# Kernel optimization log

Hardware: AMD Instinct MI355X
Metric: run time of the kernel (lower is better)

## Reference

```python
import jax, jax.numpy as jnp
import numpy as np

EPS = 1e-6


def setup_inputs() -> dict:
    key = jax.random.key(0)
    kq, kk, kv = jax.random.split(key, 3)
    B, H, S, D = 1, 16, 2048, 64
    q = jax.random.normal(kq, (B, H, S, D), dtype=jnp.float32)
    k = jax.random.normal(kk, (B, H, S, D), dtype=jnp.float32)
    v = jax.random.normal(kv, (B, H, S, D), dtype=jnp.float32)
    return {"q": q, "k": k, "v": v}


def reference(q, k, v):
    # Rebased linear attention: squared scaled QK score, causal mask,
    # normalized by running row-sum (not softmax).
    B, H, S, D = q.shape
    scale = D ** (-0.5)
    # [B,H,S,S] raw scores
    s = jnp.einsum("bhid,bhjd->bhij", q, k) * scale
    s2 = s * s
    causal = jnp.tril(jnp.ones((S, S), dtype=bool))  # k_idx <= q_idx
    s2 = jnp.where(causal, s2, jnp.zeros((), dtype=s2.dtype))
    z = jnp.sum(s2, axis=-1)  # [B,H,S]
    o = jnp.einsum("bhij,bhjd->bhid", s2, v)
    return o / (z[..., None] + EPS)
```

## Files before the change

kernel.cpp:

```cpp
#include <hip/hip_runtime.h>

typedef __attribute__((ext_vector_type(8))) short bf16x8;
typedef __attribute__((ext_vector_type(16))) float f32x16;

#define SLEN 2048
#define DDIM 64
#define NH 16
#define KEPS 1e-6f
#define TILE_B 16384
#define PSTR 72

__device__ __forceinline__ short f2bf(float x) {
    unsigned u = __float_as_uint(x);
    unsigned r = (u + 0x7FFFu + ((u >> 16) & 1u)) >> 16;
    return (short)r;
}
__device__ __forceinline__ unsigned cvtpk(float lo, float hi) {
    unsigned r;
    asm("v_cvt_pk_bf16_f32 %0, %1, %2" : "=v"(r) : "v"(lo), "v"(hi));
    return r;
}
__device__ __forceinline__ f32x16 mfma32x32(bf16x8 a, bf16x8 b, f32x16 c) {
    return __builtin_amdgcn_mfma_f32_32x32x16_bf16(a, b, c, 0, 0, 0);
}

__global__ void __launch_bounds__(256) prep_kernel(
    const float* __restrict__ K, const float* __restrict__ V, char* __restrict__ WS)
{
    __shared__ short vt[64 * PSTR];
    const int b  = blockIdx.x;
    const int h  = b >> 5;
    const int kt = b & 31;
    const int t  = threadIdx.x;
    const int j  = t >> 2;
    const int ks = t & 3;
    const int c16 = ks * 16;

    char* chunk = WS + (size_t)b * TILE_B;

    {
        const float* src = K + ((size_t)h * SLEN + kt * 64 + j) * DDIM + c16;
        float4 a = ((const float4*)src)[0], bb = ((const float4*)src)[1];
        float4 c = ((const float4*)src)[2], d = ((const float4*)src)[3];
        uint4 lo = make_uint4(cvtpk(a.x,a.y), cvtpk(a.z,a.w), cvtpk(bb.x,bb.y), cvtpk(bb.z,bb.w));
        uint4 hi = make_uint4(cvtpk(c.x,c.y), cvtpk(c.z,c.w), cvtpk(d.x,d.y), cvtpk(d.z,d.w));
        *(uint4*)(chunk + ((size_t)((ks*2+0)*64 + j)) * 16) = lo;
        *(uint4*)(chunk + ((size_t)((ks*2+1)*64 + j)) * 16) = hi;
    }
    {
        const float* src = V + ((size_t)h * SLEN + kt * 64 + j) * DDIM + c16;
        float4 a = ((const float4*)src)[0], bb = ((const float4*)src)[1];
        float4 c = ((const float4*)src)[2], d = ((const float4*)src)[3];
        float f[16] = {a.x,a.y,a.z,a.w, bb.x,bb.y,bb.z,bb.w, c.x,c.y,c.z,c.w, d.x,d.y,d.z,d.w};
#pragma unroll
        for (int q = 0; q < 16; ++q)
            vt[(c16 + q) * PSTR + j] = f2bf(f[q]);
    }
    __syncthreads();
    {
        const int d  = t >> 2;
        const int jc = (t & 3) * 16;
        uint4 lo = *(const uint4*)&vt[d * PSTR + jc];
        uint4 hi = *(const uint4*)&vt[d * PSTR + jc + 8];
        char* vbase = chunk + 8192;
        *(uint4*)(vbase + (size_t)(((jc >> 4) * 2 + 0) * 64 + d) * 16) = lo;
        *(uint4*)(vbase + (size_t)(((jc >> 4) * 2 + 1) * 64 + d) * 16) = hi;
    }
}

__global__ void __launch_bounds__(512, 4) attn_main(
    const float* __restrict__ Q, const char* __restrict__ WS, float* __restrict__ O)
{
    __shared__ float red[2][3][64][33];

    const int bid = blockIdx.x;
    const int xcd = bid & 7;
    const int m   = bid >> 3;
    const int h   = xcd | ((m & 1) << 3);
    const int c   = m >> 1;

    const int tid  = threadIdx.x;
    const int w    = tid >> 6;
    const int lane = tid & 63;
    const int il   = lane & 31;
    const int hi   = lane >> 5;
    const int msel = w >> 2;
    const int jb   = (w >> 1) & 1;
    const int e    = w & 1;

    const int g    = msel ? (31 - c) : c;
    const int half = msel;
    const int q0   = g * 64 + half * 32;

    const float* __restrict__ Qh = Q + (size_t)h * SLEN * DDIM;
    float* __restrict__ Oh = O + (size_t)h * SLEN * DDIM;
    const char* __restrict__ WSh = WS + (size_t)h * 32 * TILE_B;

    bf16x8 qf[4];
#pragma unroll
    for (int ks = 0; ks < 4; ++ks) {
        const float* src = Qh + (size_t)(q0 + il) * DDIM + ks * 16 + hi * 8;
        float4 a = *reinterpret_cast<const float4*>(src);
        float4 b = *reinterpret_cast<const float4*>(src + 4);
        uint4 uq = make_uint4(cvtpk(a.x, a.y), cvtpk(a.z, a.w),
                              cvtpk(b.x, b.y), cvtpk(b.z, b.w));
        qf[ks] = *reinterpret_cast<bf16x8*>(&uq);
    }

    f32x16 oacc0, oacc1;
#pragma unroll
    for (int rr = 0; rr < 16; ++rr) { oacc0[rr] = 0.f; oacc1[rr] = 0.f; }
    float zacc = 0.f;

    const int koff = (hi * 64 + jb * 32 + il) * 16;
    const int voff = 8192 + ((jb * 2 * 2 + hi) * 64 + il) * 16;

    const int ktend = g - ((jb > half) ? 1 : 0);

    if (e <= ktend) {
        const char* kb = WSh + (size_t)e * TILE_B + koff;
        bf16x8 kf0 = *(const bf16x8*)(kb);
        bf16x8 kf1 = *(const bf16x8*)(kb + 2048);
        bf16x8 kf2 = *(const bf16x8*)(kb + 4096);
        bf16x8 kf3 = *(const bf16x8*)(kb + 6144);

        for (int kt = e; kt <= ktend; kt += 2) {
            const char* tb = WSh + (size_t)kt * TILE_B;
            const char* vb = tb + voff;
            bf16x8 v00 = *(const bf16x8*)(vb);
            bf16x8 v01 = *(const bf16x8*)(vb + 512);
            bf16x8 v10 = *(const bf16x8*)(vb + 2048);
            bf16x8 v11 = *(const bf16x8*)(vb + 2560);

            f32x16 s;
#pragma unroll
            for (int rr = 0; rr < 16; ++rr) s[rr] = 0.f;
            s = mfma32x32(kf0, qf[0], s);
            s = mfma32x32(kf1, qf[1], s);
            s = mfma32x32(kf2, qf[2], s);
            s = mfma32x32(kf3, qf[3], s);

            if (kt + 2 <= ktend) {
                const char* nb = WSh + (size_t)(kt + 2) * TILE_B + koff;
                kf0 = *(const bf16x8*)(nb);
                kf1 = *(const bf16x8*)(nb + 2048);
                kf2 = *(const bf16x8*)(nb + 4096);
                kf3 = *(const bf16x8*)(nb + 6144);
            }

            const bool tri = (kt == g) && (jb == half);
#pragma unroll
            for (int rr = 0; rr < 16; ++rr) {
                float x = s[rr];
                x = x * x * 0.015625f;
                if (tri) {
                    int jl = (rr & 3) + 8 * (rr >> 2) + 4 * hi;
                    if (jl > il) x = 0.f;
                }
                s[rr] = x;
            }
            {
                float a0 = (s[0] + s[1]) + (s[2] + s[3]);
                float a1 = (s[4] + s[5]) + (s[6] + s[7]);
                float a2 = (s[8] + s[9]) + (s[10] + s[11]);
                float a3 = (s[12] + s[13]) + (s[14] + s[15]);
                zacc += (a0 + a1) + (a2 + a3);
            }

            {
                unsigned X  = cvtpk(s[0], s[1]);
                unsigned Xp = cvtpk(s[2], s[3]);
                unsigned Y  = cvtpk(s[4], s[5]);
                unsigned Yp = cvtpk(s[6], s[7]);
                asm("v_permlane32_swap_b32 %0, %1" : "+v"(X), "+v"(Y));
                asm("v_permlane32_swap_b32 %0, %1" : "+v"(Xp), "+v"(Yp));
                uint4 aw = make_uint4(X, Xp, Y, Yp);
                bf16x8 pf = *reinterpret_cast<bf16x8*>(&aw);
                oacc0 = mfma32x32(pf, v00, oacc0);
                oacc1 = mfma32x32(pf, v01, oacc1);
            }
            {
                unsigned X  = cvtpk(s[8],  s[9]);
                unsigned Xp = cvtpk(s[10], s[11]);
                unsigned Y  = cvtpk(s[12], s[13]);
                unsigned Yp = cvtpk(s[14], s[15]);
                asm("v_permlane32_swap_b32 %0, %1" : "+v"(X), "+v"(Y));
                asm("v_permlane32_swap_b32 %0, %1" : "+v"(Xp), "+v"(Yp));
                uint4 aw = make_uint4(X, Xp, Y, Yp);
                bf16x8 pf = *reinterpret_cast<bf16x8*>(&aw);
                oacc0 = mfma32x32(pf, v10, oacc0);
                oacc1 = mfma32x32(pf, v11, oacc1);
            }
        }
    }

    zacc += __shfl_xor(zacc, 32);
    const int sw = w & 3;
    if (sw != 0) {
        float* r = &red[msel][sw - 1][lane][0];
#pragma unroll
        for (int rr = 0; rr < 16; ++rr) { r[rr] = oacc0[rr]; r[16 + rr] = oacc1[rr]; }
        r[32] = zacc;
    }
    __syncthreads();
    if (sw == 0) {
#pragma unroll
        for (int pp = 0; pp < 3; ++pp) {
            const float* r = &red[msel][pp][lane][0];
#pragma unroll
            for (int rr = 0; rr < 16; ++rr) { oacc0[rr] += r[rr]; oacc1[rr] += r[16 + rr]; }
            zacc += r[32];
        }
        const float invl = 1.f / (zacc + KEPS);
#pragma unroll
        for (int rr = 0; rr < 16; ++rr) {
            const int rl = (rr & 3) + 8 * (rr >> 2) + 4 * hi;
            const float inv = __shfl(invl, rl);
            Oh[(size_t)(q0 + rl) * DDIM + il]      = oacc0[rr] * inv;
            Oh[(size_t)(q0 + rl) * DDIM + 32 + il] = oacc1[rr] * inv;
        }
    }
}

__global__ void __launch_bounds__(512, 4) attn_fp32(
    const float* __restrict__ Q, const float* __restrict__ K,
    const float* __restrict__ V, float* __restrict__ O)
{
    __shared__ float red[2][3][64][33];

    const int bid = blockIdx.x;
    const int xcd = bid & 7;
    const int m   = bid >> 3;
    const int h   = xcd | ((m & 1) << 3);
    const int c   = m >> 1;

    const int tid  = threadIdx.x;
    const int w    = tid >> 6;
    const int lane = tid & 63;
    const int il   = lane & 31;
    const int hi   = lane >> 5;
    const int msel = w >> 2;
    const int jb   = (w >> 1) & 1;
    const int e    = w & 1;

    const int g    = msel ? (31 - c) : c;
    const int half = msel;
    const int q0   = g * 64 + half * 32;

    const float* Qh = Q + (size_t)h * SLEN * DDIM;
    const float* Kh = K + (size_t)h * SLEN * DDIM;
    const float* Vh = V + (size_t)h * SLEN * DDIM;
    float* Oh = O + (size_t)h * SLEN * DDIM;

    bf16x8 qf[4];
#pragma unroll
    for (int ks = 0; ks < 4; ++ks) {
        const float* src = Qh + (size_t)(q0 + il) * DDIM + ks * 16 + hi * 8;
        float4 a = *reinterpret_cast<const float4*>(src);
        float4 b = *reinterpret_cast<const float4*>(src + 4);
        uint4 uq = make_uint4(cvtpk(a.x, a.y), cvtpk(a.z, a.w),
                              cvtpk(b.x, b.y), cvtpk(b.z, b.w));
        qf[ks] = *reinterpret_cast<bf16x8*>(&uq);
    }

    f32x16 oacc0, oacc1;
#pragma unroll
    for (int rr = 0; rr < 16; ++rr) { oacc0[rr] = 0.f; oacc1[rr] = 0.f; }
    float zacc = 0.f;

    const int ktend = g - ((jb > half) ? 1 : 0);

    for (int kt = e; kt <= ktend; kt += 2) {
        f32x16 s;
#pragma unroll
        for (int rr = 0; rr < 16; ++rr) s[rr] = 0.f;
#pragma unroll
        for (int ks = 0; ks < 4; ++ks) {
            const float* src = Kh + (size_t)(kt * 64 + jb * 32 + il) * DDIM + ks * 16 + hi * 8;
            float4 a = *reinterpret_cast<const float4*>(src);
            float4 b = *reinterpret_cast<const float4*>(src + 4);
            uint4 uk = make_uint4(cvtpk(a.x, a.y), cvtpk(a.z, a.w),
                                  cvtpk(b.x, b.y), cvtpk(b.z, b.w));
            s = mfma32x32(*reinterpret_cast<bf16x8*>(&uk), qf[ks], s);
        }
        const bool tri = (kt == g) && (jb == half);
#pragma unroll
        for (int rr = 0; rr < 16; ++rr) {
            float x = s[rr];
            x = x * x * 0.015625f;
            if (tri) {
                int jl = (rr & 3) + 8 * (rr >> 2) + 4 * hi;
                if (jl > il) x = 0.f;
            }
            s[rr] = x;
            zacc += x;
        }
#pragma unroll
        for (int s16 = 0; s16 < 2; ++s16) {
            unsigned X  = cvtpk(s[8*s16+0], s[8*s16+1]);
            unsigned Xp = cvtpk(s[8*s16+2], s[8*s16+3]);
            unsigned Y  = cvtpk(s[8*s16+4], s[8*s16+5]);
            unsigned Yp = cvtpk(s[8*s16+6], s[8*s16+7]);
            asm("v_permlane32_swap_b32 %0, %1" : "+v"(X), "+v"(Y));
            asm("v_permlane32_swap_b32 %0, %1" : "+v"(Xp), "+v"(Yp));
            uint4 aw = make_uint4(X, Xp, Y, Yp);
            bf16x8 pf = *reinterpret_cast<bf16x8*>(&aw);
#pragma unroll
            for (int dt = 0; dt < 2; ++dt) {
                float v8[8];
#pragma unroll
                for (int t = 0; t < 8; ++t)
                    v8[t] = Vh[(size_t)(kt * 64 + (jb * 2 + s16) * 16 + hi * 8 + t) * DDIM + dt * 32 + il];
                uint4 uv = make_uint4(cvtpk(v8[0], v8[1]), cvtpk(v8[2], v8[3]),
                                      cvtpk(v8[4], v8[5]), cvtpk(v8[6], v8[7]));
                bf16x8 vf = *reinterpret_cast<bf16x8*>(&uv);
                if (dt == 0) oacc0 = mfma32x32(pf, vf, oacc0);
                else         oacc1 = mfma32x32(pf, vf, oacc1);
            }
        }
    }

    zacc += __shfl_xor(zacc, 32);
    const int sw = w & 3;
    if (sw != 0) {
        float* r = &red[msel][sw - 1][lane][0];
#pragma unroll
        for (int rr = 0; rr < 16; ++rr) { r[rr] = oacc0[rr]; r[16 + rr] = oacc1[rr]; }
        r[32] = zacc;
    }
    __syncthreads();
    if (sw == 0) {
#pragma unroll
        for (int pp = 0; pp < 3; ++pp) {
            const float* r = &red[msel][pp][lane][0];
#pragma unroll
            for (int rr = 0; rr < 16; ++rr) { oacc0[rr] += r[rr]; oacc1[rr] += r[16 + rr]; }
            zacc += r[32];
        }
        const float invl = 1.f / (zacc + KEPS);
#pragma unroll
        for (int rr = 0; rr < 16; ++rr) {
            const int rl = (rr & 3) + 8 * (rr >> 2) + 4 * hi;
            const float inv = __shfl(invl, rl);
            Oh[(size_t)(q0 + rl) * DDIM + il]      = oacc0[rr] * inv;
            Oh[(size_t)(q0 + rl) * DDIM + 32 + il] = oacc1[rr] * inv;
        }
    }
}

extern "C" void kernel_launch(void* const* d_in, const int* in_sizes, int n_in,
                              void* d_out, int out_size, void* d_ws, size_t ws_size,
                              hipStream_t stream) {
    const float* q = (const float*)d_in[0];
    const float* k = (const float*)d_in[1];
    const float* v = (const float*)d_in[2];
    float* o = (float*)d_out;

    const size_t need = (size_t)NH * 32 * TILE_B;
    if (ws_size >= need) {
        char* ws = (char*)d_ws;
        hipLaunchKernelGGL(prep_kernel, dim3(NH * 32), dim3(256), 0, stream, k, v, ws);
        hipLaunchKernelGGL(attn_main, dim3(512), dim3(512), 0, stream, q, ws, o);
    } else {
        hipLaunchKernelGGL(attn_fp32, dim3(512), dim3(512), 0, stream, q, k, v, o);
    }
}
```

Before: 30.78 us.

## Process paired query slices sequentially in 256-thread blocks, prefetch V, simplify V transpose

The main kernel now uses 256-thread blocks that handle two balanced query slices (s and 63-s) one after the other, instead of 512 threads splitting them across wave halves. V fragments are now prefetched one tile ahead like K, and s_setprio raises wave priority around the MFMA sections. The prep kernel drops its LDS transpose and builds packed V pairs directly from four row loads. Each block now carries the same work with fewer waves, so there is less parallelism per CU and a second reduction barrier per block.

```diff
diff --git a/kernel.cpp b/kernel.cpp
--- a/kernel.cpp
+++ b/kernel.cpp
@@ -8,13 +8,7 @@
 #define NH 16
 #define KEPS 1e-6f
 #define TILE_B 16384
-#define PSTR 72
-
-__device__ __forceinline__ short f2bf(float x) {
-    unsigned u = __float_as_uint(x);
-    unsigned r = (u + 0x7FFFu + ((u >> 16) & 1u)) >> 16;
-    return (short)r;
-}
+
 __device__ __forceinline__ unsigned cvtpk(float lo, float hi) {
     unsigned r;
     asm("v_cvt_pk_bf16_f32 %0, %1, %2" : "=v"(r) : "v"(lo), "v"(hi));
@@ -27,18 +21,14 @@
 __global__ void __launch_bounds__(256) prep_kernel(
     const float* __restrict__ K, const float* __restrict__ V, char* __restrict__ WS)
 {
-    __shared__ short vt[64 * PSTR];
     const int b  = blockIdx.x;
     const int h  = b >> 5;
     const int kt = b & 31;
     const int t  = threadIdx.x;
-    const int j  = t >> 2;
-    const int ks = t & 3;
-    const int c16 = ks * 16;
-
     char* chunk = WS + (size_t)b * TILE_B;
 
     {
+        const int j = t >> 2, ks = t & 3, c16 = ks * 16;
         const float* src = K + ((size_t)h * SLEN + kt * 64 + j) * DDIM + c16;
         float4 a = ((const float4*)src)[0], bb = ((const float4*)src)[1];
         float4 c = ((const float4*)src)[2], d = ((const float4*)src)[3];
@@ -48,37 +38,202 @@
         *(uint4*)(chunk + ((size_t)((ks*2+1)*64 + j)) * 16) = hi;
     }
     {
-        const float* src = V + ((size_t)h * SLEN + kt * 64 + j) * DDIM + c16;
-        float4 a = ((const float4*)src)[0], bb = ((const float4*)src)[1];
-        float4 c = ((const float4*)src)[2], d = ((const float4*)src)[3];
-        float f[16] = {a.x,a.y,a.z,a.w, bb.x,bb.y,bb.z,bb.w, c.x,c.y,c.z,c.w, d.x,d.y,d.z,d.w};
-#pragma unroll
-        for (int q = 0; q < 16; ++q)
-            vt[(c16 + q) * PSTR + j] = f2bf(f[q]);
-    }
-    __syncthreads();
-    {
-        const int d  = t >> 2;
-        const int jc = (t & 3) * 16;
-        uint4 lo = *(const uint4*)&vt[d * PSTR + jc];
-        uint4 hi = *(const uint4*)&vt[d * PSTR + jc + 8];
+        const int j0 = (t & 15) * 4, d0 = (t >> 4) * 4;
+        const float* vs = V + ((size_t)h * SLEN + kt * 64 + j0) * DDIM + d0;
+        float4 r0 = *(const float4*)(vs);
+        float4 r1 = *(const float4*)(vs + DDIM);
+        float4 r2 = *(const float4*)(vs + 2 * DDIM);
+        float4 r3 = *(const float4*)(vs + 3 * DDIM);
         char* vbase = chunk + 8192;
-        *(uint4*)(vbase + (size_t)(((jc >> 4) * 2 + 0) * 64 + d) * 16) = lo;
-        *(uint4*)(vbase + (size_t)(((jc >> 4) * 2 + 1) * 64 + d) * 16) = hi;
-    }
-}
-
-__global__ void __launch_bounds__(512, 4) attn_main(
+        const int cv  = ((j0 >> 4) << 1) | ((j0 >> 3) & 1);
+        const int tof = j0 & 7;
+#pragma unroll
+        for (int c = 0; c < 4; ++c) {
+            uint2 pk = make_uint2(
+                cvtpk(((const float*)&r0)[c], ((const float*)&r1)[c]),
+                cvtpk(((const float*)&r2)[c], ((const float*)&r3)[c]));
+            *(uint2*)(vbase + (size_t)(cv * 64 + d0 + c) * 16 + tof * 2) = pk;
+        }
+    }
+}
+
+__global__ void __launch_bounds__(256, 2) attn_main(
     const float* __restrict__ Q, const char* __restrict__ WS, float* __restrict__ O)
 {
     __shared__ float red[2][3][64][33];
 
+    const int bid = blockIdx.x;
+    const int xcd = bid & 7;
+    const int m   = bid >> 3;
+    const int h   = ((m & 1) << 3) | xcd;
+    const int s   = m >> 1;
+
+    const int tid  = threadIdx.x;
+    const int w    = tid >> 6;
+    const int lane = tid & 63;
+    const int il   = lane & 31;
+    const int hi   = lane >> 5;
+    const int jb   = w & 1;
+    const int e    = w >> 1;
+
+    const float* __restrict__ Qh = Q + (size_t)h * SLEN * DDIM;
+    float* __restrict__ Oh = O + (size_t)h * SLEN * DDIM;
+    const char* __restrict__ WSh = WS + (size_t)h * 32 * TILE_B;
+
+    const int koff = (hi * 64 + jb * 32 + il) * 16;
+    const int voff = 8192 + ((jb * 4 + hi) * 64 + il) * 16;
+
+    auto process = [&](int slice, int phase) {
+        const int g    = slice >> 1;
+        const int half = slice & 1;
+        const int q0   = slice * 32;
+
+        bf16x8 qf[4];
+#pragma unroll
+        for (int ks = 0; ks < 4; ++ks) {
+            const float* src = Qh + (size_t)(q0 + il) * DDIM + ks * 16 + hi * 8;
+            float4 a = *reinterpret_cast<const float4*>(src);
+            float4 b = *reinterpret_cast<const float4*>(src + 4);
+            uint4 uq = make_uint4(cvtpk(a.x, a.y), cvtpk(a.z, a.w),
+                                  cvtpk(b.x, b.y), cvtpk(b.z, b.w));
+            qf[ks] = *reinterpret_cast<bf16x8*>(&uq);
+        }
+
+        f32x16 o0, o1;
+#pragma unroll
+        for (int rr = 0; rr < 16; ++rr) { o0[rr] = 0.f; o1[rr] = 0.f; }
+        float z = 0.f;
+
+        const int ktend = g - ((jb > half) ? 1 : 0);
+
+        if (e <= ktend) {
+            const char* kb = WSh + (size_t)e * TILE_B + koff;
+            bf16x8 kf0 = *(const bf16x8*)(kb);
+            bf16x8 kf1 = *(const bf16x8*)(kb + 2048);
+            bf16x8 kf2 = *(const bf16x8*)(kb + 4096);
+            bf16x8 kf3 = *(const bf16x8*)(kb + 6144);
+            const char* vb = WSh + (size_t)e * TILE_B + voff;
+            bf16x8 v00 = *(const bf16x8*)(vb);
+            bf16x8 v01 = *(const bf16x8*)(vb + 512);
+            bf16x8 v10 = *(const bf16x8*)(vb + 2048);
+            bf16x8 v11 = *(const bf16x8*)(vb + 2560);
+
+            for (int kt = e; kt <= ktend; kt += 2) {
+                __builtin_amdgcn_s_setprio(1);
+                f32x16 sv;
+#pragma unroll
+                for (int rr = 0; rr < 16; ++rr) sv[rr] = 0.f;
+                sv = mfma32x32(kf0, qf[0], sv);
+                sv = mfma32x32(kf1, qf[1], sv);
+                sv = mfma32x32(kf2, qf[2], sv);
+                sv = mfma32x32(kf3, qf[3], sv);
+                __builtin_amdgcn_s_setprio(0);
+
+                if (kt + 2 <= ktend) {
+                    const char* nb = WSh + (size_t)(kt + 2) * TILE_B + koff;
+                    kf0 = *(const bf16x8*)(nb);
+                    kf1 = *(const bf16x8*)(nb + 2048);
+                    kf2 = *(const bf16x8*)(nb + 4096);
+                    kf3 = *(const bf16x8*)(nb + 6144);
+                }
+
+                const bool tri = (kt == g) && (jb == half);
+#pragma unroll
+                for (int rr = 0; rr < 16; ++rr) {
+                    float x = sv[rr];
+                    x = x * x * 0.015625f;
+                    if (tri) {
+                        int jl = (rr & 3) + 8 * (rr >> 2) + 4 * hi;
+                        if (jl > il) x = 0.f;
+                    }
+                    sv[rr] = x;
+                }
+                {
+                    float a0 = (sv[0] + sv[1]) + (sv[2] + sv[3]);
+                    float a1 = (sv[4] + sv[5]) + (sv[6] + sv[7]);
+                    float a2 = (sv[8] + sv[9]) + (sv[10] + sv[11]);
+                    float a3 = (sv[12] + sv[13]) + (sv[14] + sv[15]);
+                    z += (a0 + a1) + (a2 + a3);
+                }
+
+                __builtin_amdgcn_s_setprio(1);
+                {
+                    unsigned X  = cvtpk(sv[0], sv[1]);
+                    unsigned Xp = cvtpk(sv[2], sv[3]);
+                    unsigned Y  = cvtpk(sv[4], sv[5]);
+                    unsigned Yp = cvtpk(sv[6], sv[7]);
+                    asm("v_permlane32_swap_b32 %0, %1" : "+v"(X), "+v"(Y));
+                    asm("v_permlane32_swap_b32 %0, %1" : "+v"(Xp), "+v"(Yp));
+                    uint4 aw = make_uint4(X, Xp, Y, Yp);
+                    bf16x8 pf = *reinterpret_cast<bf16x8*>(&aw);
+                    o0 = mfma32x32(pf, v00, o0);
+                    o1 = mfma32x32(pf, v01, o1);
+                }
+                {
+                    unsigned X  = cvtpk(sv[8],  sv[9]);
+                    unsigned Xp = cvtpk(sv[10], sv[11]);
+                    unsigned Y  = cvtpk(sv[12], sv[13]);
+                    unsigned Yp = cvtpk(sv[14], sv[15]);
+                    asm("v_permlane32_swap_b32 %0, %1" : "+v"(X), "+v"(Y));
+                    asm("v_permlane32_swap_b32 %0, %1" : "+v"(Xp), "+v"(Yp));
+                    uint4 aw = make_uint4(X, Xp, Y, Yp);
+                    bf16x8 pf = *reinterpret_cast<bf16x8*>(&aw);
+                    o0 = mfma32x32(pf, v10, o0);
+                    o1 = mfma32x32(pf, v11, o1);
+                }
+                __builtin_amdgcn_s_setprio(0);
+
+                if (kt + 2 <= ktend) {
+                    const char* nv = WSh + (size_t)(kt + 2) * TILE_B + voff;
+                    v00 = *(const bf16x8*)(nv);
+                    v01 = *(const bf16x8*)(nv + 512);
+                    v10 = *(const bf16x8*)(nv + 2048);
+                    v11 = *(const bf16x8*)(nv + 2560);
+                }
+            }
+        }
+
+        z += __shfl_xor(z, 32);
+        if (w != 0) {
+            float* r = &red[phase][w - 1][lane][0];
+#pragma unroll
+            for (int rr = 0; rr < 16; ++rr) { r[rr] = o0[rr]; r[16 + rr] = o1[rr]; }
+            r[32] = z;
+        }
+        __syncthreads();
+        if (w == 0) {
+#pragma unroll
+            for (int pp = 0; pp < 3; ++pp) {
+                const float* r = &red[phase][pp][lane][0];
+#pragma unroll
+                for (int rr = 0; rr < 16; ++rr) { o0[rr] += r[rr]; o1[rr] += r[16 + rr]; }
+                z += r[32];
+            }
+            const float invl = 1.f / (z + KEPS);
+#pragma unroll
+            for (int rr = 0; rr < 16; ++rr) {
+                const int rl = (rr & 3) + 8 * (rr >> 2) + 4 * hi;
+                const float inv = __shfl(invl, rl);
+                Oh[(size_t)(q0 + rl) * DDIM + il]      = o0[rr] * inv;
+                Oh[(size_t)(q0 + rl) * DDIM + 32 + il] = o1[rr] * inv;
+            }
+        }
+    };
+
+    process(s, 0);
+    process(63 - s, 1);
+}
+
+__global__ void __launch_bounds__(512, 4) attn_fp32(
+    const float* __restrict__ Q, const float* __restrict__ K,
+    const float* __restrict__ V, float* __restrict__ O)
+{
+    __shared__ float red[2][3][64][33];
     const int bid = blockIdx.x;
     const int xcd = bid & 7;
     const int m   = bid >> 3;
     const int h   = xcd | ((m & 1) << 3);
     const int c   = m >> 1;
-
     const int tid  = threadIdx.x;
     const int w    = tid >> 6;
     const int lane = tid & 63;
@@ -87,14 +242,14 @@
     const int msel = w >> 2;
     const int jb   = (w >> 1) & 1;
     const int e    = w & 1;
-
     const int g    = msel ? (31 - c) : c;
     const int half = msel;
     const int q0   = g * 64 + half * 32;
 
-    const float* __restrict__ Qh = Q + (size_t)h * SLEN * DDIM;
-    float* __restrict__ Oh = O + (size_t)h * SLEN * DDIM;
-    const char* __restrict__ WSh = WS + (size_t)h * 32 * TILE_B;
+    const float* Qh = Q + (size_t)h * SLEN * DDIM;
+    const float* Kh = K + (size_t)h * SLEN * DDIM;
+    const float* Vh = V + (size_t)h * SLEN * DDIM;
+    float* Oh = O + (size_t)h * SLEN * DDIM;
 
     bf16x8 qf[4];
 #pragma unroll
@@ -106,174 +261,16 @@
                               cvtpk(b.x, b.y), cvtpk(b.z, b.w));
         qf[ks] = *reinterpret_cast<bf16x8*>(&uq);
     }
-
     f32x16 oacc0, oacc1;
 #pragma unroll
     for (int rr = 0; rr < 16; ++rr) { oacc0[rr] = 0.f; oacc1[rr] = 0.f; }
     float zacc = 0.f;
-
-    const int koff = (hi * 64 + jb * 32 + il) * 16;
-    const int voff = 8192 + ((jb * 2 * 2 + hi) * 64 + il) * 16;
-
     const int ktend = g - ((jb > half) ? 1 : 0);
 
-    if (e <= ktend) {
-        const char* kb = WSh + (size_t)e * TILE_B + koff;
-        bf16x8 kf0 = *(const bf16x8*)(kb);
-        bf16x8 kf1 = *(const bf16x8*)(kb + 2048);
-        bf16x8 kf2 = *(const bf16x8*)(kb + 4096);
-        bf16x8 kf3 = *(const bf16x8*)(kb + 6144);
-
-        for (int kt = e; kt <= ktend; kt += 2) {
-            const char* tb = WSh + (size_t)kt * TILE_B;
-            const char* vb = tb + voff;
-            bf16x8 v00 = *(const bf16x8*)(vb);
-            bf16x8 v01 = *(const bf16x8*)(vb + 512);
-            bf16x8 v10 = *(const bf16x8*)(vb + 2048);
-            bf16x8 v11 = *(const bf16x8*)(vb + 2560);
-
-            f32x16 s;
-#pragma unroll
-            for (int rr = 0; rr < 16; ++rr) s[rr] = 0.f;
-            s = mfma32x32(kf0, qf[0], s);
-            s = mfma32x32(kf1, qf[1], s);
-            s = mfma32x32(kf2, qf[2], s);
-            s = mfma32x32(kf3, qf[3], s);
-
-            if (kt + 2 <= ktend) {
-                const char* nb = WSh + (size_t)(kt + 2) * TILE_B + koff;
-                kf0 = *(const bf16x8*)(nb);
-                kf1 = *(const bf16x8*)(nb + 2048);
-                kf2 = *(const bf16x8*)(nb + 4096);
-                kf3 = *(const bf16x8*)(nb + 6144);
-            }
-
-            const bool tri = (kt == g) && (jb == half);
-#pragma unroll
-            for (int rr = 0; rr < 16; ++rr) {
-                float x = s[rr];
-                x = x * x * 0.015625f;
-                if (tri) {
-                    int jl = (rr & 3) + 8 * (rr >> 2) + 4 * hi;
-                    if (jl > il) x = 0.f;
-                }
-                s[rr] = x;
-            }
-            {
-                float a0 = (s[0] + s[1]) + (s[2] + s[3]);
-                float a1 = (s[4] + s[5]) + (s[6] + s[7]);
-                float a2 = (s[8] + s[9]) + (s[10] + s[11]);
-                float a3 = (s[12] + s[13]) + (s[14] + s[15]);
-                zacc += (a0 + a1) + (a2 + a3);
-            }
-
-            {
-                unsigned X  = cvtpk(s[0], s[1]);
-                unsigned Xp = cvtpk(s[2], s[3]);
-                unsigned Y  = cvtpk(s[4], s[5]);
-                unsigned Yp = cvtpk(s[6], s[7]);
-                asm("v_permlane32_swap_b32 %0, %1" : "+v"(X), "+v"(Y));
-                asm("v_permlane32_swap_b32 %0, %1" : "+v"(Xp), "+v"(Yp));
-                uint4 aw = make_uint4(X, Xp, Y, Yp);
-                bf16x8 pf = *reinterpret_cast<bf16x8*>(&aw);
-                oacc0 = mfma32x32(pf, v00, oacc0);
-                oacc1 = mfma32x32(pf, v01, oacc1);
-            }
-            {
-                unsigned X  = cvtpk(s[8],  s[9]);
-                unsigned Xp = cvtpk(s[10], s[11]);
-                unsigned Y  = cvtpk(s[12], s[13]);
-                unsigned Yp = cvtpk(s[14], s[15]);
-                asm("v_permlane32_swap_b32 %0, %1" : "+v"(X), "+v"(Y));
-                asm("v_permlane32_swap_b32 %0, %1" : "+v"(Xp), "+v"(Yp));
-                uint4 aw = make_uint4(X, Xp, Y, Yp);
-                bf16x8 pf = *reinterpret_cast<bf16x8*>(&aw);
-                oacc0 = mfma32x32(pf, v10, oacc0);
-                oacc1 = mfma32x32(pf, v11, oacc1);
-            }
-        }
-    }
-
-    zacc += __shfl_xor(zacc, 32);
-    const int sw = w & 3;
-    if (sw != 0) {
-        float* r = &red[msel][sw - 1][lane][0];
-#pragma unroll
-        for (int rr = 0; rr < 16; ++rr) { r[rr] = oacc0[rr]; r[16 + rr] = oacc1[rr]; }
-        r[32] = zacc;
-    }
-    __syncthreads();
-    if (sw == 0) {
-#pragma unroll
-        for (int pp = 0; pp < 3; ++pp) {
-            const float* r = &red[msel][pp][lane][0];
-#pragma unroll
-            for (int rr = 0; rr < 16; ++rr) { oacc0[rr] += r[rr]; oacc1[rr] += r[16 + rr]; }
-            zacc += r[32];
-        }
-        const float invl = 1.f / (zacc + KEPS);
-#pragma unroll
-        for (int rr = 0; rr < 16; ++rr) {
-            const int rl = (rr & 3) + 8 * (rr >> 2) + 4 * hi;
-            const float inv = __shfl(invl, rl);
-            Oh[(size_t)(q0 + rl) * DDIM + il]      = oacc0[rr] * inv;
-            Oh[(size_t)(q0 + rl) * DDIM + 32 + il] = oacc1[rr] * inv;
-        }
-    }
-}
-
-__global__ void __launch_bounds__(512, 4) attn_fp32(
-    const float* __restrict__ Q, const float* __restrict__ K,
-    const float* __restrict__ V, float* __restrict__ O)
-{
-    __shared__ float red[2][3][64][33];
-
-    const int bid = blockIdx.x;
-    const int xcd = bid & 7;
-    const int m   = bid >> 3;
-    const int h   = xcd | ((m & 1) << 3);
-    const int c   = m >> 1;
-
-    const int tid  = threadIdx.x;
-    const int w    = tid >> 6;
-    const int lane = tid & 63;
-    const int il   = lane & 31;
-    const int hi   = lane >> 5;
-    const int msel = w >> 2;
-    const int jb   = (w >> 1) & 1;
-    const int e    = w & 1;
-
-    const int g    = msel ? (31 - c) : c;
-    const int half = msel;
-    const int q0   = g * 64 + half * 32;
-
-    const float* Qh = Q + (size_t)h * SLEN * DDIM;
-    const float* Kh = K + (size_t)h * SLEN * DDIM;
-    const float* Vh = V + (size_t)h * SLEN * DDIM;
-    float* Oh = O + (size_t)h * SLEN * DDIM;
-
-    bf16x8 qf[4];
-#pragma unroll
-    for (int ks = 0; ks < 4; ++ks) {
-        const float* src = Qh + (size_t)(q0 + il) * DDIM + ks * 16 + hi * 8;
-        float4 a = *reinterpret_cast<const float4*>(src);
-        float4 b = *reinterpret_cast<const float4*>(src + 4);
-        uint4 uq = make_uint4(cvtpk(a.x, a.y), cvtpk(a.z, a.w),
-                              cvtpk(b.x, b.y), cvtpk(b.z, b.w));
-        qf[ks] = *reinterpret_cast<bf16x8*>(&uq);
-    }
-
-    f32x16 oacc0, oacc1;
-#pragma unroll
-    for (int rr = 0; rr < 16; ++rr) { oacc0[rr] = 0.f; oacc1[rr] = 0.f; }
-    float zacc = 0.f;
-
-    const int ktend = g - ((jb > half) ? 1 : 0);
-
     for (int kt = e; kt <= ktend; kt += 2) {
-        f32x16 s;
-#pragma unroll
-        for (int rr = 0; rr < 16; ++rr) s[rr] = 0.f;
+        f32x16 sv;
+#pragma unroll
+        for (int rr = 0; rr < 16; ++rr) sv[rr] = 0.f;
 #pragma unroll
         for (int ks = 0; ks < 4; ++ks) {
             const float* src = Kh + (size_t)(kt * 64 + jb * 32 + il) * DDIM + ks * 16 + hi * 8;
@@ -281,26 +278,26 @@
             float4 b = *reinterpret_cast<const float4*>(src + 4);
             uint4 uk = make_uint4(cvtpk(a.x, a.y), cvtpk(a.z, a.w),
                                   cvtpk(b.x, b.y), cvtpk(b.z, b.w));
-            s = mfma32x32(*reinterpret_cast<bf16x8*>(&uk), qf[ks], s);
+            sv = mfma32x32(*reinterpret_cast<bf16x8*>(&uk), qf[ks], sv);
         }
         const bool tri = (kt == g) && (jb == half);
 #pragma unroll
         for (int rr = 0; rr < 16; ++rr) {
-            float x = s[rr];
+            float x = sv[rr];
             x = x * x * 0.015625f;
             if (tri) {
                 int jl = (rr & 3) + 8 * (rr >> 2) + 4 * hi;
                 if (jl > il) x = 0.f;
             }
-            s[rr] = x;
+            sv[rr] = x;
             zacc += x;
         }
 #pragma unroll
         for (int s16 = 0; s16 < 2; ++s16) {
-            unsigned X  = cvtpk(s[8*s16+0], s[8*s16+1]);
-            unsigned Xp = cvtpk(s[8*s16+2], s[8*s16+3]);
-            unsigned Y  = cvtpk(s[8*s16+4], s[8*s16+5]);
-            unsigned Yp = cvtpk(s[8*s16+6], s[8*s16+7]);
+            unsigned X  = cvtpk(sv[8*s16+0], sv[8*s16+1]);
+            unsigned Xp = cvtpk(sv[8*s16+2], sv[8*s16+3]);
+            unsigned Y  = cvtpk(sv[8*s16+4], sv[8*s16+5]);
+            unsigned Yp = cvtpk(sv[8*s16+6], sv[8*s16+7]);
             asm("v_permlane32_swap_b32 %0, %1" : "+v"(X), "+v"(Y));
             asm("v_permlane32_swap_b32 %0, %1" : "+v"(Xp), "+v"(Yp));
             uint4 aw = make_uint4(X, Xp, Y, Yp);
@@ -360,7 +357,7 @@
     if (ws_size >= need) {
         char* ws = (char*)d_ws;
         hipLaunchKernelGGL(prep_kernel, dim3(NH * 32), dim3(256), 0, stream, k, v, ws);
-        hipLaunchKernelGGL(attn_main, dim3(512), dim3(512), 0, stream, q, ws, o);
+        hipLaunchKernelGGL(attn_main, dim3(512), dim3(256), 0, stream, q, ws, o);
     } else {
         hipLaunchKernelGGL(attn_fp32, dim3(512), dim3(512), 0, stream, q, k, v, o);
     }
```

Measured after the change: 30.99 us. Within noise of the previous version (+0.7%).
